# Kernel optimization log

Hardware: AMD Instinct MI355X
Metric: run time of the kernel (lower is better)

Reference implementation:

```python
import jax, jax.numpy as jnp
import numpy as np

B, F_SIZE, DIM = 2048, 32, 64
LAYER_SIZES = (128, 128)


def setup_inputs() -> dict:
    key = jax.random.key(0)
    k1, k2, k3 = jax.random.split(key, 3)
    inputs = jax.random.normal(k1, (B, F_SIZE, DIM), dtype=jnp.float32)
    # Conv1d(kernel=1) weights: (out_channels, in_channels)
    W0 = jax.random.normal(k2, (128, F_SIZE * F_SIZE), dtype=jnp.float32) * 0.03
    b0 = jnp.zeros((128,), dtype=jnp.float32)
    # split_half -> field_nums[1] = 64 -> in_channels = 64 * 32 = 2048
    W1 = jax.random.normal(k3, (128, 64 * F_SIZE), dtype=jnp.float32) * 0.03
    b1 = jnp.zeros((128,), dtype=jnp.float32)
    return {"inputs": inputs, "W0": W0, "b0": b0, "W1": W1, "b1": b1}


def _cin_forward(inputs, Ws, bs):
    batch, _, dim = inputs.shape
    x0 = inputs
    h = inputs
    finals = []
    n_layers = len(Ws)
    for i in range(n_layers):
        H = h.shape[1]
        M = x0.shape[1]
        # outer-product interaction: (b, H, M, d) -> (b, H*M, d)
        z = jnp.einsum('bhd,bmd->bhmd', h, x0).reshape(batch, H * M, dim)
        # 1x1 conv == per-position channel matmul
        out = jnp.einsum('bcd,oc->bod', z, Ws[i]) + bs[i][None, :, None]
        out = jax.nn.relu(out)
        size = Ws[i].shape[0]
        if i != n_layers - 1:
            # split_half: first half feeds next layer, second half is output
            h = out[:, : size // 2, :]
            finals.append(out[:, size // 2 :, :])
        else:
            finals.append(out)
    result = jnp.concatenate(finals, axis=1)  # (b, 64 + 128, d)
    return jnp.sum(result, axis=-1)           # (b, 192)


def reference(inputs, W0, b0, W1, b1):
    return _cin_forward(inputs, (W0, W1), (b0, b1))
```

## Files before the change

kernel.cpp:

```cpp
#include <hip/hip_runtime.h>


#define K0 1024
#define K1 2048
#define OUTC 192
#define L0_ELEMS (128 * K0)
#define L1_ELEMS (128 * K1)
#define L0_FRAGS (L0_ELEMS / 8)
#define L1_FRAGS (L1_ELEMS / 8)

typedef _Float16 v8h  __attribute__((ext_vector_type(8)));
typedef _Float16 v2h  __attribute__((ext_vector_type(2)));
typedef float    v16f __attribute__((ext_vector_type(16)));

__global__ void convert_w_kernel(const float* __restrict__ W0,
                                 const float* __restrict__ W1,
                                 _Float16* __restrict__ wsw) {
    int t = blockIdx.x * blockDim.x + threadIdx.x;
    if (t >= L0_FRAGS + L1_FRAGS) return;
    const float* src;
    _Float16* dst;
    if (t < L0_FRAGS) {
        int lane = t & 63, rt = (t >> 6) & 3, ks = t >> 8;
        int row = rt * 32 + (lane & 31);
        int k   = ks * 16 + (lane >> 5) * 8;
        src = W0 + (size_t)row * K0 + k;
        dst = wsw + (size_t)t * 8;
    } else {
        int u = t - L0_FRAGS;
        int lane = u & 63, rt = (u >> 6) & 3, ks = u >> 8;
        int row = rt * 32 + (lane & 31);
        int k   = ks * 16 + (lane >> 5) * 8;
        src = W1 + (size_t)row * K1 + k;
        dst = wsw + L0_ELEMS + (size_t)u * 8;
    }
    #pragma unroll
    for (int j = 0; j < 8; ++j) dst[j] = (_Float16)src[j];
}

__device__ __forceinline__ v8h dupscalar(uint32_t u) {
    uint32_t pair = (u << 16) | u;
    v2h p = __builtin_bit_cast(v2h, pair);
    return __builtin_shufflevector(p, p, 0, 1, 0, 1, 0, 1, 0, 1);
}

__global__ __launch_bounds__(256, 4) void cin_kernel(
    const float* __restrict__ X,
    const float* __restrict__ b0,
    const float* __restrict__ b1,
    const _Float16* __restrict__ Wsw,
    float* __restrict__ out)
{
    __shared__ uint16_t xS[2][32 * 64];
    __shared__ uint16_t h1S[2][64 * 64];
    __shared__ float biasLds[256];

    const int tid  = threadIdx.x;
    const int wave = tid >> 6;
    const int lane = tid & 63;
    const int bi   = wave >> 1;
    const int rw   = wave & 1;
    const int l31  = lane & 31;
    const int hi   = lane >> 5;
    const size_t bb = (size_t)blockIdx.x * 2;

    if (tid < 128) biasLds[tid] = b0[tid];
    else           biasLds[tid] = b1[tid - 128];

    const float* xsrc = X + bb * 2048;
    for (int i = tid; i < 4096; i += 256) {
        int bby = i >> 11, loc = i & 2047;
        int m = loc >> 6, d = loc & 63;
        _Float16 h = (_Float16)xsrc[i];
        ((_Float16*)&h1S[bby][0])[d * 40 + m] = h;
        xS[bby][m * 64 + d] = __builtin_bit_cast(uint16_t, h);
    }
    __syncthreads();

    v8h xv[2][2];
    {
        const _Float16* xT = (const _Float16*)&h1S[bi][0];
        #pragma unroll
        for (int c = 0; c < 2; ++c)
            #pragma unroll
            for (int p = 0; p < 2; ++p)
                xv[c][p] = *(const v8h*)&xT[(c * 32 + l31) * 40 + p * 16 + hi * 8];
    }
    __syncthreads();

    v16f acc[2][2];
    #pragma unroll
    for (int rt = 0; rt < 2; ++rt)
        #pragma unroll
        for (int c = 0; c < 2; ++c) acc[rt][c] = (v16f)0.0f;

    {
        const _Float16* Wp = Wsw + (size_t)rw * 1024 + (size_t)lane * 8;
        #pragma unroll 2
        for (int h = 0; h < 32; ++h) {
            v8h a00 = *(const v8h*)(Wp);
            v8h a10 = *(const v8h*)(Wp + 512);
            v8h a01 = *(const v8h*)(Wp + 2048);
            v8h a11 = *(const v8h*)(Wp + 2560);
            Wp += 4096;
            uint32_t u0 = xS[bi][h * 64 + l31];
            uint32_t u1 = xS[bi][h * 64 + 32 + l31];
            v8h s80 = dupscalar(u0), s81 = dupscalar(u1);
            v8h b00 = s80 * xv[0][0];
            acc[0][0] = __builtin_amdgcn_mfma_f32_32x32x16_f16(a00, b00, acc[0][0], 0, 0, 0);
            acc[1][0] = __builtin_amdgcn_mfma_f32_32x32x16_f16(a10, b00, acc[1][0], 0, 0, 0);
            v8h b10 = s81 * xv[1][0];
            acc[0][1] = __builtin_amdgcn_mfma_f32_32x32x16_f16(a00, b10, acc[0][1], 0, 0, 0);
            acc[1][1] = __builtin_amdgcn_mfma_f32_32x32x16_f16(a10, b10, acc[1][1], 0, 0, 0);
            v8h b01 = s80 * xv[0][1];
            acc[0][0] = __builtin_amdgcn_mfma_f32_32x32x16_f16(a01, b01, acc[0][0], 0, 0, 0);
            acc[1][0] = __builtin_amdgcn_mfma_f32_32x32x16_f16(a11, b01, acc[1][0], 0, 0, 0);
            v8h b11 = s81 * xv[1][1];
            acc[0][1] = __builtin_amdgcn_mfma_f32_32x32x16_f16(a01, b11, acc[0][1], 0, 0, 0);
            acc[1][1] = __builtin_amdgcn_mfma_f32_32x32x16_f16(a11, b11, acc[1][1], 0, 0, 0);
        }
    }

    if (rw == 0) {
        #pragma unroll
        for (int rt = 0; rt < 2; ++rt)
            #pragma unroll
            for (int reg = 0; reg < 16; ++reg) {
                int row = rt * 32 + (reg & 3) + 8 * (reg >> 2) + 4 * hi;
                float bias = biasLds[row];
                #pragma unroll
                for (int c = 0; c < 2; ++c) {
                    float v = acc[rt][c][reg] + bias;
                    v = v > 0.0f ? v : 0.0f;
                    h1S[bi][row * 64 + c * 32 + l31] =
                        __builtin_bit_cast(uint16_t, (_Float16)v);
                }
            }
    } else {
        #pragma unroll
        for (int rt = 0; rt < 2; ++rt)
            #pragma unroll
            for (int reg = 0; reg < 16; ++reg) {
                int grow = 64 + rt * 32 + (reg & 3) + 8 * (reg >> 2) + 4 * hi;
                float bias = biasLds[grow];
                float v0 = acc[rt][0][reg] + bias;
                float v1 = acc[rt][1][reg] + bias;
                float s = (v0 > 0.0f ? v0 : 0.0f) + (v1 > 0.0f ? v1 : 0.0f);
                s += __shfl_xor(s, 1);
                s += __shfl_xor(s, 2);
                s += __shfl_xor(s, 4);
                s += __shfl_xor(s, 8);
                s += __shfl_xor(s, 16);
                if (l31 == 0) out[(bb + bi) * OUTC + (grow - 64)] = s;
            }
    }
    __syncthreads();

    #pragma unroll
    for (int rt = 0; rt < 2; ++rt)
        #pragma unroll
        for (int c = 0; c < 2; ++c) acc[rt][c] = (v16f)0.0f;

    {
        const _Float16* Wp = Wsw + L0_ELEMS + (size_t)rw * 1024 + (size_t)lane * 8;
        #pragma unroll 2
        for (int h = 0; h < 64; ++h) {
            v8h a00 = *(const v8h*)(Wp);
            v8h a10 = *(const v8h*)(Wp + 512);
            v8h a01 = *(const v8h*)(Wp + 2048);
            v8h a11 = *(const v8h*)(Wp + 2560);
            Wp += 4096;
            uint32_t u0 = h1S[bi][h * 64 + l31];
            uint32_t u1 = h1S[bi][h * 64 + 32 + l31];
            v8h s80 = dupscalar(u0), s81 = dupscalar(u1);
            v8h b00 = s80 * xv[0][0];
            acc[0][0] = __builtin_amdgcn_mfma_f32_32x32x16_f16(a00, b00, acc[0][0], 0, 0, 0);
            acc[1][0] = __builtin_amdgcn_mfma_f32_32x32x16_f16(a10, b00, acc[1][0], 0, 0, 0);
            v8h b10 = s81 * xv[1][0];
            acc[0][1] = __builtin_amdgcn_mfma_f32_32x32x16_f16(a00, b10, acc[0][1], 0, 0, 0);
            acc[1][1] = __builtin_amdgcn_mfma_f32_32x32x16_f16(a10, b10, acc[1][1], 0, 0, 0);
            v8h b01 = s80 * xv[0][1];
            acc[0][0] = __builtin_amdgcn_mfma_f32_32x32x16_f16(a01, b01, acc[0][0], 0, 0, 0);
            acc[1][0] = __builtin_amdgcn_mfma_f32_32x32x16_f16(a11, b01, acc[1][0], 0, 0, 0);
            v8h b11 = s81 * xv[1][1];
            acc[0][1] = __builtin_amdgcn_mfma_f32_32x32x16_f16(a01, b11, acc[0][1], 0, 0, 0);
            acc[1][1] = __builtin_amdgcn_mfma_f32_32x32x16_f16(a11, b11, acc[1][1], 0, 0, 0);
        }
    }

    #pragma unroll
    for (int rt = 0; rt < 2; ++rt)
        #pragma unroll
        for (int reg = 0; reg < 16; ++reg) {
            int grow = rw * 64 + rt * 32 + (reg & 3) + 8 * (reg >> 2) + 4 * hi;
            float bias = biasLds[128 + grow];
            float v0 = acc[rt][0][reg] + bias;
            float v1 = acc[rt][1][reg] + bias;
            float s = (v0 > 0.0f ? v0 : 0.0f) + (v1 > 0.0f ? v1 : 0.0f);
            s += __shfl_xor(s, 1);
            s += __shfl_xor(s, 2);
            s += __shfl_xor(s, 4);
            s += __shfl_xor(s, 8);
            s += __shfl_xor(s, 16);
            if (l31 == 0) out[(bb + bi) * OUTC + 64 + grow] = s;
        }
}

extern "C" void kernel_launch(void* const* d_in, const int* in_sizes, int n_in,
                              void* d_out, int out_size, void* d_ws, size_t ws_size,
                              hipStream_t stream) {
    const float* X  = (const float*)d_in[0];
    const float* W0 = (const float*)d_in[1];
    const float* b0 = (const float*)d_in[2];
    const float* W1 = (const float*)d_in[3];
    const float* b1 = (const float*)d_in[4];
    float* out = (float*)d_out;
    _Float16* wsw = (_Float16*)d_ws;

    convert_w_kernel<<<(L0_FRAGS + L1_FRAGS + 255) / 256, 256, 0, stream>>>(W0, W1, wsw);
    cin_kernel<<<1024, 256, 0, stream>>>(X, b0, b1, wsw, out);
}
```

Measured before the change: 175.1 us.

## Process one batch per block with waves split by row tile and prefetch weights

Changes the work split from two batch items per block (each handled by two waves over 64 rows) to one batch item per block, with the four waves each owning a 32-row tile. Each wave now holds two accumulators instead of four. Weight fragments and LDS scalars are software-pipelined two iterations ahead in registers. This doubles the grid and halves per-wave accumulator registers, aiming for more parallelism and latency hiding. In exchange, each weight fragment is reused across only one batch item instead of two, which increases global/L2 weight traffic per output.

```diff
diff --git a/kernel.cpp b/kernel.cpp
--- a/kernel.cpp
+++ b/kernel.cpp
@@ -44,6 +44,8 @@
     return __builtin_shufflevector(p, p, 0, 1, 0, 1, 0, 1, 0, 1);
 }
 
+#define MFMA32(A, B, C) __builtin_amdgcn_mfma_f32_32x32x16_f16((A), (B), (C), 0, 0, 0)
+
 __global__ __launch_bounds__(256, 4) void cin_kernel(
     const float* __restrict__ X,
     const float* __restrict__ b0,
@@ -51,35 +53,32 @@
     const _Float16* __restrict__ Wsw,
     float* __restrict__ out)
 {
-    __shared__ uint16_t xS[2][32 * 64];
-    __shared__ uint16_t h1S[2][64 * 64];
+    __shared__ uint16_t xS[32 * 64];
+    __shared__ uint16_t h1S[64 * 64];
     __shared__ float biasLds[256];
 
     const int tid  = threadIdx.x;
     const int wave = tid >> 6;
     const int lane = tid & 63;
-    const int bi   = wave >> 1;
-    const int rw   = wave & 1;
     const int l31  = lane & 31;
     const int hi   = lane >> 5;
-    const size_t bb = (size_t)blockIdx.x * 2;
+    const size_t b = blockIdx.x;
 
     if (tid < 128) biasLds[tid] = b0[tid];
     else           biasLds[tid] = b1[tid - 128];
 
-    const float* xsrc = X + bb * 2048;
-    for (int i = tid; i < 4096; i += 256) {
-        int bby = i >> 11, loc = i & 2047;
-        int m = loc >> 6, d = loc & 63;
+    const float* xsrc = X + b * 2048;
+    for (int i = tid; i < 2048; i += 256) {
+        int m = i >> 6, d = i & 63;
         _Float16 h = (_Float16)xsrc[i];
-        ((_Float16*)&h1S[bby][0])[d * 40 + m] = h;
-        xS[bby][m * 64 + d] = __builtin_bit_cast(uint16_t, h);
+        ((_Float16*)h1S)[d * 40 + m] = h;
+        xS[m * 64 + d] = __builtin_bit_cast(uint16_t, h);
     }
     __syncthreads();
 
     v8h xv[2][2];
     {
-        const _Float16* xT = (const _Float16*)&h1S[bi][0];
+        const _Float16* xT = (const _Float16*)h1S;
         #pragma unroll
         for (int c = 0; c < 2; ++c)
             #pragma unroll
@@ -88,122 +87,110 @@
     }
     __syncthreads();
 
-    v16f acc[2][2];
-    #pragma unroll
-    for (int rt = 0; rt < 2; ++rt)
-        #pragma unroll
-        for (int c = 0; c < 2; ++c) acc[rt][c] = (v16f)0.0f;
-
+    v16f acc0 = (v16f)0.0f, acc1 = (v16f)0.0f;
     {
-        const _Float16* Wp = Wsw + (size_t)rw * 1024 + (size_t)lane * 8;
+        const _Float16* Wb = Wsw + (size_t)wave * 512 + (size_t)lane * 8;
+        v8h Ap0 = *(const v8h*)(Wb);
+        v8h Ap1 = *(const v8h*)(Wb + 2048);
+        v8h Bp0 = *(const v8h*)(Wb + 4096);
+        v8h Bp1 = *(const v8h*)(Wb + 4096 + 2048);
+        uint32_t ua0 = xS[l31],      ua1 = xS[32 + l31];
+        uint32_t ub0 = xS[64 + l31], ub1 = xS[64 + 32 + l31];
         #pragma unroll 2
         for (int h = 0; h < 32; ++h) {
-            v8h a00 = *(const v8h*)(Wp);
-            v8h a10 = *(const v8h*)(Wp + 512);
-            v8h a01 = *(const v8h*)(Wp + 2048);
-            v8h a11 = *(const v8h*)(Wp + 2560);
-            Wp += 4096;
-            uint32_t u0 = xS[bi][h * 64 + l31];
-            uint32_t u1 = xS[bi][h * 64 + 32 + l31];
-            v8h s80 = dupscalar(u0), s81 = dupscalar(u1);
+            int hn = (h + 2 < 32) ? h + 2 : 31;
+            v8h P0 = *(const v8h*)(Wb + (size_t)hn * 4096);
+            v8h P1 = *(const v8h*)(Wb + (size_t)hn * 4096 + 2048);
+            uint32_t w0 = xS[hn * 64 + l31];
+            uint32_t w1 = xS[hn * 64 + 32 + l31];
+            v8h s80 = dupscalar(ua0), s81 = dupscalar(ua1);
             v8h b00 = s80 * xv[0][0];
-            acc[0][0] = __builtin_amdgcn_mfma_f32_32x32x16_f16(a00, b00, acc[0][0], 0, 0, 0);
-            acc[1][0] = __builtin_amdgcn_mfma_f32_32x32x16_f16(a10, b00, acc[1][0], 0, 0, 0);
             v8h b10 = s81 * xv[1][0];
-            acc[0][1] = __builtin_amdgcn_mfma_f32_32x32x16_f16(a00, b10, acc[0][1], 0, 0, 0);
-            acc[1][1] = __builtin_amdgcn_mfma_f32_32x32x16_f16(a10, b10, acc[1][1], 0, 0, 0);
+            acc0 = MFMA32(Ap0, b00, acc0);
+            acc1 = MFMA32(Ap0, b10, acc1);
             v8h b01 = s80 * xv[0][1];
-            acc[0][0] = __builtin_amdgcn_mfma_f32_32x32x16_f16(a01, b01, acc[0][0], 0, 0, 0);
-            acc[1][0] = __builtin_amdgcn_mfma_f32_32x32x16_f16(a11, b01, acc[1][0], 0, 0, 0);
             v8h b11 = s81 * xv[1][1];
-            acc[0][1] = __builtin_amdgcn_mfma_f32_32x32x16_f16(a01, b11, acc[0][1], 0, 0, 0);
-            acc[1][1] = __builtin_amdgcn_mfma_f32_32x32x16_f16(a11, b11, acc[1][1], 0, 0, 0);
-        }
-    }
-
-    if (rw == 0) {
+            acc0 = MFMA32(Ap1, b01, acc0);
+            acc1 = MFMA32(Ap1, b11, acc1);
+            Ap0 = Bp0; Ap1 = Bp1; Bp0 = P0; Bp1 = P1;
+            ua0 = ub0; ua1 = ub1; ub0 = w0; ub1 = w1;
+        }
+    }
+
+    if (wave < 2) {
         #pragma unroll
-        for (int rt = 0; rt < 2; ++rt)
-            #pragma unroll
-            for (int reg = 0; reg < 16; ++reg) {
-                int row = rt * 32 + (reg & 3) + 8 * (reg >> 2) + 4 * hi;
-                float bias = biasLds[row];
-                #pragma unroll
-                for (int c = 0; c < 2; ++c) {
-                    float v = acc[rt][c][reg] + bias;
-                    v = v > 0.0f ? v : 0.0f;
-                    h1S[bi][row * 64 + c * 32 + l31] =
-                        __builtin_bit_cast(uint16_t, (_Float16)v);
-                }
-            }
+        for (int reg = 0; reg < 16; ++reg) {
+            int row = wave * 32 + (reg & 3) + 8 * (reg >> 2) + 4 * hi;
+            float bias = biasLds[row];
+            float v0 = acc0[reg] + bias;
+            float v1 = acc1[reg] + bias;
+            v0 = v0 > 0.0f ? v0 : 0.0f;
+            v1 = v1 > 0.0f ? v1 : 0.0f;
+            h1S[row * 64 + l31]      = __builtin_bit_cast(uint16_t, (_Float16)v0);
+            h1S[row * 64 + 32 + l31] = __builtin_bit_cast(uint16_t, (_Float16)v1);
+        }
     } else {
         #pragma unroll
-        for (int rt = 0; rt < 2; ++rt)
-            #pragma unroll
-            for (int reg = 0; reg < 16; ++reg) {
-                int grow = 64 + rt * 32 + (reg & 3) + 8 * (reg >> 2) + 4 * hi;
-                float bias = biasLds[grow];
-                float v0 = acc[rt][0][reg] + bias;
-                float v1 = acc[rt][1][reg] + bias;
-                float s = (v0 > 0.0f ? v0 : 0.0f) + (v1 > 0.0f ? v1 : 0.0f);
-                s += __shfl_xor(s, 1);
-                s += __shfl_xor(s, 2);
-                s += __shfl_xor(s, 4);
-                s += __shfl_xor(s, 8);
-                s += __shfl_xor(s, 16);
-                if (l31 == 0) out[(bb + bi) * OUTC + (grow - 64)] = s;
-            }
-    }
-    __syncthreads();
-
-    #pragma unroll
-    for (int rt = 0; rt < 2; ++rt)
-        #pragma unroll
-        for (int c = 0; c < 2; ++c) acc[rt][c] = (v16f)0.0f;
-
-    {
-        const _Float16* Wp = Wsw + L0_ELEMS + (size_t)rw * 1024 + (size_t)lane * 8;
-        #pragma unroll 2
-        for (int h = 0; h < 64; ++h) {
-            v8h a00 = *(const v8h*)(Wp);
-            v8h a10 = *(const v8h*)(Wp + 512);
-            v8h a01 = *(const v8h*)(Wp + 2048);
-            v8h a11 = *(const v8h*)(Wp + 2560);
-            Wp += 4096;
-            uint32_t u0 = h1S[bi][h * 64 + l31];
-            uint32_t u1 = h1S[bi][h * 64 + 32 + l31];
-            v8h s80 = dupscalar(u0), s81 = dupscalar(u1);
-            v8h b00 = s80 * xv[0][0];
-            acc[0][0] = __builtin_amdgcn_mfma_f32_32x32x16_f16(a00, b00, acc[0][0], 0, 0, 0);
-            acc[1][0] = __builtin_amdgcn_mfma_f32_32x32x16_f16(a10, b00, acc[1][0], 0, 0, 0);
-            v8h b10 = s81 * xv[1][0];
-            acc[0][1] = __builtin_amdgcn_mfma_f32_32x32x16_f16(a00, b10, acc[0][1], 0, 0, 0);
-            acc[1][1] = __builtin_amdgcn_mfma_f32_32x32x16_f16(a10, b10, acc[1][1], 0, 0, 0);
-            v8h b01 = s80 * xv[0][1];
-            acc[0][0] = __builtin_amdgcn_mfma_f32_32x32x16_f16(a01, b01, acc[0][0], 0, 0, 0);
-            acc[1][0] = __builtin_amdgcn_mfma_f32_32x32x16_f16(a11, b01, acc[1][0], 0, 0, 0);
-            v8h b11 = s81 * xv[1][1];
-            acc[0][1] = __builtin_amdgcn_mfma_f32_32x32x16_f16(a01, b11, acc[0][1], 0, 0, 0);
-            acc[1][1] = __builtin_amdgcn_mfma_f32_32x32x16_f16(a11, b11, acc[1][1], 0, 0, 0);
-        }
-    }
-
-    #pragma unroll
-    for (int rt = 0; rt < 2; ++rt)
-        #pragma unroll
         for (int reg = 0; reg < 16; ++reg) {
-            int grow = rw * 64 + rt * 32 + (reg & 3) + 8 * (reg >> 2) + 4 * hi;
-            float bias = biasLds[128 + grow];
-            float v0 = acc[rt][0][reg] + bias;
-            float v1 = acc[rt][1][reg] + bias;
+            int grow = wave * 32 + (reg & 3) + 8 * (reg >> 2) + 4 * hi;
+            float bias = biasLds[grow];
+            float v0 = acc0[reg] + bias;
+            float v1 = acc1[reg] + bias;
             float s = (v0 > 0.0f ? v0 : 0.0f) + (v1 > 0.0f ? v1 : 0.0f);
             s += __shfl_xor(s, 1);
             s += __shfl_xor(s, 2);
             s += __shfl_xor(s, 4);
             s += __shfl_xor(s, 8);
             s += __shfl_xor(s, 16);
-            if (l31 == 0) out[(bb + bi) * OUTC + 64 + grow] = s;
-        }
+            if (l31 == 0) out[b * OUTC + (grow - 64)] = s;
+        }
+    }
+    __syncthreads();
+
+    acc0 = (v16f)0.0f; acc1 = (v16f)0.0f;
+    {
+        const _Float16* Wb = Wsw + L0_ELEMS + (size_t)wave * 512 + (size_t)lane * 8;
+        v8h Ap0 = *(const v8h*)(Wb);
+        v8h Ap1 = *(const v8h*)(Wb + 2048);
+        v8h Bp0 = *(const v8h*)(Wb + 4096);
+        v8h Bp1 = *(const v8h*)(Wb + 4096 + 2048);
+        uint32_t ua0 = h1S[l31],      ua1 = h1S[32 + l31];
+        uint32_t ub0 = h1S[64 + l31], ub1 = h1S[64 + 32 + l31];
+        #pragma unroll 2
+        for (int h = 0; h < 64; ++h) {
+            int hn = (h + 2 < 64) ? h + 2 : 63;
+            v8h P0 = *(const v8h*)(Wb + (size_t)hn * 4096);
+            v8h P1 = *(const v8h*)(Wb + (size_t)hn * 4096 + 2048);
+            uint32_t w0 = h1S[hn * 64 + l31];
+            uint32_t w1 = h1S[hn * 64 + 32 + l31];
+            v8h s80 = dupscalar(ua0), s81 = dupscalar(ua1);
+            v8h b00 = s80 * xv[0][0];
+            v8h b10 = s81 * xv[1][0];
+            acc0 = MFMA32(Ap0, b00, acc0);
+            acc1 = MFMA32(Ap0, b10, acc1);
+            v8h b01 = s80 * xv[0][1];
+            v8h b11 = s81 * xv[1][1];
+            acc0 = MFMA32(Ap1, b01, acc0);
+            acc1 = MFMA32(Ap1, b11, acc1);
+            Ap0 = Bp0; Ap1 = Bp1; Bp0 = P0; Bp1 = P1;
+            ua0 = ub0; ua1 = ub1; ub0 = w0; ub1 = w1;
+        }
+    }
+
+    #pragma unroll
+    for (int reg = 0; reg < 16; ++reg) {
+        int grow = wave * 32 + (reg & 3) + 8 * (reg >> 2) + 4 * hi;
+        float bias = biasLds[128 + grow];
+        float v0 = acc0[reg] + bias;
+        float v1 = acc1[reg] + bias;
+        float s = (v0 > 0.0f ? v0 : 0.0f) + (v1 > 0.0f ? v1 : 0.0f);
+        s += __shfl_xor(s, 1);
+        s += __shfl_xor(s, 2);
+        s += __shfl_xor(s, 4);
+        s += __shfl_xor(s, 8);
+        s += __shfl_xor(s, 16);
+        if (l31 == 0) out[b * OUTC + 64 + grow] = s;
+    }
 }
 
 extern "C" void kernel_launch(void* const* d_in, const int* in_sizes, int n_in,
@@ -218,5 +205,5 @@
     _Float16* wsw = (_Float16*)d_ws;
 
     convert_w_kernel<<<(L0_FRAGS + L1_FRAGS + 255) / 256, 256, 0, stream>>>(W0, W1, wsw);
-    cin_kernel<<<1024, 256, 0, stream>>>(X, b0, b1, wsw, out);
-}
+    cin_kernel<<<2048, 256, 0, stream>>>(X, b0, b1, wsw, out);
+}
```

New measurement: 177.6 us. About the same (+1.4%).

## Process two batch samples per wave to reuse weight fragments, prefetch next iteration

Applied to the files above, without the earlier changes.

Each block now handles four batch samples instead of two, and each wave computes two samples so every weight fragment loaded from global memory feeds twice as many MFMAs. The K loops are software-pipelined so the next iteration's weight and LDS scalar loads are issued before the current MFMAs. The conversion kernel is reindexed to read source rows contiguously. Accumulator registers double and launch bounds drop to 2 blocks per SIMD, so occupancy falls and the grid is halved.

```diff
diff --git a/kernel.cpp b/kernel.cpp
--- a/kernel.cpp
+++ b/kernel.cpp
@@ -6,8 +6,6 @@
 #define OUTC 192
 #define L0_ELEMS (128 * K0)
 #define L1_ELEMS (128 * K1)
-#define L0_FRAGS (L0_ELEMS / 8)
-#define L1_FRAGS (L1_ELEMS / 8)
 
 typedef _Float16 v8h  __attribute__((ext_vector_type(8)));
 typedef _Float16 v2h  __attribute__((ext_vector_type(2)));
@@ -16,26 +14,23 @@
 __global__ void convert_w_kernel(const float* __restrict__ W0,
                                  const float* __restrict__ W1,
                                  _Float16* __restrict__ wsw) {
-    int t = blockIdx.x * blockDim.x + threadIdx.x;
-    if (t >= L0_FRAGS + L1_FRAGS) return;
+    size_t i = ((size_t)blockIdx.x * blockDim.x + threadIdx.x) * 8;
+    if (i >= (size_t)(L0_ELEMS + L1_ELEMS)) return;
     const float* src;
-    _Float16* dst;
-    if (t < L0_FRAGS) {
-        int lane = t & 63, rt = (t >> 6) & 3, ks = t >> 8;
-        int row = rt * 32 + (lane & 31);
-        int k   = ks * 16 + (lane >> 5) * 8;
-        src = W0 + (size_t)row * K0 + k;
-        dst = wsw + (size_t)t * 8;
+    _Float16* dstbase;
+    int K, local;
+    if (i < L0_ELEMS) {
+        K = K0; src = W0; dstbase = wsw; local = (int)i;
     } else {
-        int u = t - L0_FRAGS;
-        int lane = u & 63, rt = (u >> 6) & 3, ks = u >> 8;
-        int row = rt * 32 + (lane & 31);
-        int k   = ks * 16 + (lane >> 5) * 8;
-        src = W1 + (size_t)row * K1 + k;
-        dst = wsw + L0_ELEMS + (size_t)u * 8;
-    }
-    #pragma unroll
-    for (int j = 0; j < 8; ++j) dst[j] = (_Float16)src[j];
+        K = K1; src = W1; dstbase = wsw + L0_ELEMS; local = (int)(i - L0_ELEMS);
+    }
+    int row = local / K, k = local % K;
+    int ks = k >> 4, oct = (k >> 3) & 1;
+    int frag = ks * 256 + (row >> 5) * 64 + oct * 32 + (row & 31);
+    const float* s = src + (size_t)row * K + k;
+    _Float16* d = dstbase + (size_t)frag * 8;
+    #pragma unroll
+    for (int j = 0; j < 8; ++j) d[j] = (_Float16)s[j];
 }
 
 __device__ __forceinline__ v8h dupscalar(uint32_t u) {
@@ -44,31 +39,34 @@
     return __builtin_shufflevector(p, p, 0, 1, 0, 1, 0, 1, 0, 1);
 }
 
-__global__ __launch_bounds__(256, 4) void cin_kernel(
+#define MFMA32(A, B, C) __builtin_amdgcn_mfma_f32_32x32x16_f16((A), (B), (C), 0, 0, 0)
+
+__global__ __launch_bounds__(256, 2) void cin_kernel(
     const float* __restrict__ X,
     const float* __restrict__ b0,
     const float* __restrict__ b1,
     const _Float16* __restrict__ Wsw,
     float* __restrict__ out)
 {
-    __shared__ uint16_t xS[2][32 * 64];
-    __shared__ uint16_t h1S[2][64 * 64];
+    __shared__ uint16_t xS[4][2048];
+    __shared__ uint16_t h1S[4][4096];
     __shared__ float biasLds[256];
 
     const int tid  = threadIdx.x;
     const int wave = tid >> 6;
     const int lane = tid & 63;
-    const int bi   = wave >> 1;
     const int rw   = wave & 1;
+    const int bp   = wave >> 1;
+    const int lb0  = bp * 2;
     const int l31  = lane & 31;
     const int hi   = lane >> 5;
-    const size_t bb = (size_t)blockIdx.x * 2;
+    const size_t bb = (size_t)blockIdx.x * 4;
 
     if (tid < 128) biasLds[tid] = b0[tid];
     else           biasLds[tid] = b1[tid - 128];
 
     const float* xsrc = X + bb * 2048;
-    for (int i = tid; i < 4096; i += 256) {
+    for (int i = tid; i < 8192; i += 256) {
         int bby = i >> 11, loc = i & 2047;
         int m = loc >> 6, d = loc & 63;
         _Float16 h = (_Float16)xsrc[i];
@@ -77,133 +75,244 @@
     }
     __syncthreads();
 
-    v8h xv[2][2];
-    {
-        const _Float16* xT = (const _Float16*)&h1S[bi][0];
+    v8h xv[2][2][2];
+    #pragma unroll
+    for (int lb = 0; lb < 2; ++lb) {
+        const _Float16* xT = (const _Float16*)&h1S[lb0 + lb][0];
         #pragma unroll
         for (int c = 0; c < 2; ++c)
             #pragma unroll
             for (int p = 0; p < 2; ++p)
-                xv[c][p] = *(const v8h*)&xT[(c * 32 + l31) * 40 + p * 16 + hi * 8];
+                xv[lb][c][p] = *(const v8h*)&xT[(c * 32 + l31) * 40 + p * 16 + hi * 8];
     }
     __syncthreads();
 
-    v16f acc[2][2];
-    #pragma unroll
-    for (int rt = 0; rt < 2; ++rt)
-        #pragma unroll
-        for (int c = 0; c < 2; ++c) acc[rt][c] = (v16f)0.0f;
+    v16f acc[2][2][2];
+    #pragma unroll
+    for (int lb = 0; lb < 2; ++lb)
+        #pragma unroll
+        for (int rt = 0; rt < 2; ++rt)
+            #pragma unroll
+            for (int c = 0; c < 2; ++c) acc[lb][rt][c] = (v16f)0.0f;
 
     {
         const _Float16* Wp = Wsw + (size_t)rw * 1024 + (size_t)lane * 8;
+        const uint16_t* xp0 = &xS[lb0][0];
+        const uint16_t* xp1 = &xS[lb0 + 1][0];
+        v8h na00 = *(const v8h*)(Wp);
+        v8h na10 = *(const v8h*)(Wp + 512);
+        v8h na01 = *(const v8h*)(Wp + 2048);
+        v8h na11 = *(const v8h*)(Wp + 2560);
+        uint32_t nu00 = xp0[l31], nu01 = xp0[32 + l31];
+        uint32_t nu10 = xp1[l31], nu11 = xp1[32 + l31];
         #pragma unroll 2
-        for (int h = 0; h < 32; ++h) {
-            v8h a00 = *(const v8h*)(Wp);
-            v8h a10 = *(const v8h*)(Wp + 512);
-            v8h a01 = *(const v8h*)(Wp + 2048);
-            v8h a11 = *(const v8h*)(Wp + 2560);
+        for (int h = 0; h < 31; ++h) {
+            v8h a00 = na00, a10 = na10, a01 = na01, a11 = na11;
+            uint32_t u00 = nu00, u01 = nu01, u10 = nu10, u11 = nu11;
             Wp += 4096;
-            uint32_t u0 = xS[bi][h * 64 + l31];
-            uint32_t u1 = xS[bi][h * 64 + 32 + l31];
-            v8h s80 = dupscalar(u0), s81 = dupscalar(u1);
-            v8h b00 = s80 * xv[0][0];
-            acc[0][0] = __builtin_amdgcn_mfma_f32_32x32x16_f16(a00, b00, acc[0][0], 0, 0, 0);
-            acc[1][0] = __builtin_amdgcn_mfma_f32_32x32x16_f16(a10, b00, acc[1][0], 0, 0, 0);
-            v8h b10 = s81 * xv[1][0];
-            acc[0][1] = __builtin_amdgcn_mfma_f32_32x32x16_f16(a00, b10, acc[0][1], 0, 0, 0);
-            acc[1][1] = __builtin_amdgcn_mfma_f32_32x32x16_f16(a10, b10, acc[1][1], 0, 0, 0);
-            v8h b01 = s80 * xv[0][1];
-            acc[0][0] = __builtin_amdgcn_mfma_f32_32x32x16_f16(a01, b01, acc[0][0], 0, 0, 0);
-            acc[1][0] = __builtin_amdgcn_mfma_f32_32x32x16_f16(a11, b01, acc[1][0], 0, 0, 0);
-            v8h b11 = s81 * xv[1][1];
-            acc[0][1] = __builtin_amdgcn_mfma_f32_32x32x16_f16(a01, b11, acc[0][1], 0, 0, 0);
-            acc[1][1] = __builtin_amdgcn_mfma_f32_32x32x16_f16(a11, b11, acc[1][1], 0, 0, 0);
+            na00 = *(const v8h*)(Wp);
+            na10 = *(const v8h*)(Wp + 512);
+            na01 = *(const v8h*)(Wp + 2048);
+            na11 = *(const v8h*)(Wp + 2560);
+            nu00 = xp0[(h + 1) * 64 + l31];
+            nu01 = xp0[(h + 1) * 64 + 32 + l31];
+            nu10 = xp1[(h + 1) * 64 + l31];
+            nu11 = xp1[(h + 1) * 64 + 32 + l31];
+            v8h s00 = dupscalar(u00), s01 = dupscalar(u01);
+            v8h s10 = dupscalar(u10), s11 = dupscalar(u11);
+            v8h b000 = s00 * xv[0][0][0];
+            acc[0][0][0] = MFMA32(a00, b000, acc[0][0][0]);
+            acc[0][1][0] = MFMA32(a10, b000, acc[0][1][0]);
+            v8h b010 = s01 * xv[0][1][0];
+            acc[0][0][1] = MFMA32(a00, b010, acc[0][0][1]);
+            acc[0][1][1] = MFMA32(a10, b010, acc[0][1][1]);
+            v8h b100 = s10 * xv[1][0][0];
+            acc[1][0][0] = MFMA32(a00, b100, acc[1][0][0]);
+            acc[1][1][0] = MFMA32(a10, b100, acc[1][1][0]);
+            v8h b110 = s11 * xv[1][1][0];
+            acc[1][0][1] = MFMA32(a00, b110, acc[1][0][1]);
+            acc[1][1][1] = MFMA32(a10, b110, acc[1][1][1]);
+            v8h b001 = s00 * xv[0][0][1];
+            acc[0][0][0] = MFMA32(a01, b001, acc[0][0][0]);
+            acc[0][1][0] = MFMA32(a11, b001, acc[0][1][0]);
+            v8h b011 = s01 * xv[0][1][1];
+            acc[0][0][1] = MFMA32(a01, b011, acc[0][0][1]);
+            acc[0][1][1] = MFMA32(a11, b011, acc[0][1][1]);
+            v8h b101 = s10 * xv[1][0][1];
+            acc[1][0][0] = MFMA32(a01, b101, acc[1][0][0]);
+            acc[1][1][0] = MFMA32(a11, b101, acc[1][1][0]);
+            v8h b111 = s11 * xv[1][1][1];
+            acc[1][0][1] = MFMA32(a01, b111, acc[1][0][1]);
+            acc[1][1][1] = MFMA32(a11, b111, acc[1][1][1]);
         }
+        v8h s00 = dupscalar(nu00), s01 = dupscalar(nu01);
+        v8h s10 = dupscalar(nu10), s11 = dupscalar(nu11);
+        v8h b000 = s00 * xv[0][0][0];
+        acc[0][0][0] = MFMA32(na00, b000, acc[0][0][0]);
+        acc[0][1][0] = MFMA32(na10, b000, acc[0][1][0]);
+        v8h b010 = s01 * xv[0][1][0];
+        acc[0][0][1] = MFMA32(na00, b010, acc[0][0][1]);
+        acc[0][1][1] = MFMA32(na10, b010, acc[0][1][1]);
+        v8h b100 = s10 * xv[1][0][0];
+        acc[1][0][0] = MFMA32(na00, b100, acc[1][0][0]);
+        acc[1][1][0] = MFMA32(na10, b100, acc[1][1][0]);
+        v8h b110 = s11 * xv[1][1][0];
+        acc[1][0][1] = MFMA32(na00, b110, acc[1][0][1]);
+        acc[1][1][1] = MFMA32(na10, b110, acc[1][1][1]);
+        v8h b001 = s00 * xv[0][0][1];
+        acc[0][0][0] = MFMA32(na01, b001, acc[0][0][0]);
+        acc[0][1][0] = MFMA32(na11, b001, acc[0][1][0]);
+        v8h b011 = s01 * xv[0][1][1];
+        acc[0][0][1] = MFMA32(na01, b011, acc[0][0][1]);
+        acc[0][1][1] = MFMA32(na11, b011, acc[0][1][1]);
+        v8h b101 = s10 * xv[1][0][1];
+        acc[1][0][0] = MFMA32(na01, b101, acc[1][0][0]);
+        acc[1][1][0] = MFMA32(na11, b101, acc[1][1][0]);
+        v8h b111 = s11 * xv[1][1][1];
+        acc[1][0][1] = MFMA32(na01, b111, acc[1][0][1]);
+        acc[1][1][1] = MFMA32(na11, b111, acc[1][1][1]);
     }
 
     if (rw == 0) {
         #pragma unroll
+        for (int lb = 0; lb < 2; ++lb)
+            #pragma unroll
+            for (int rt = 0; rt < 2; ++rt)
+                #pragma unroll
+                for (int reg = 0; reg < 16; ++reg) {
+                    int row = rt * 32 + (reg & 3) + 8 * (reg >> 2) + 4 * hi;
+                    float bias = biasLds[row];
+                    float v0 = acc[lb][rt][0][reg] + bias;
+                    float v1 = acc[lb][rt][1][reg] + bias;
+                    v0 = v0 > 0.0f ? v0 : 0.0f;
+                    v1 = v1 > 0.0f ? v1 : 0.0f;
+                    h1S[lb0 + lb][row * 64 + l31]      = __builtin_bit_cast(uint16_t, (_Float16)v0);
+                    h1S[lb0 + lb][row * 64 + 32 + l31] = __builtin_bit_cast(uint16_t, (_Float16)v1);
+                }
+    } else {
+        #pragma unroll
+        for (int lb = 0; lb < 2; ++lb)
+            #pragma unroll
+            for (int rt = 0; rt < 2; ++rt)
+                #pragma unroll
+                for (int reg = 0; reg < 16; ++reg) {
+                    int grow = 64 + rt * 32 + (reg & 3) + 8 * (reg >> 2) + 4 * hi;
+                    float bias = biasLds[grow];
+                    float v0 = acc[lb][rt][0][reg] + bias;
+                    float v1 = acc[lb][rt][1][reg] + bias;
+                    float s = (v0 > 0.0f ? v0 : 0.0f) + (v1 > 0.0f ? v1 : 0.0f);
+                    s += __shfl_xor(s, 1);
+                    s += __shfl_xor(s, 2);
+                    s += __shfl_xor(s, 4);
+                    s += __shfl_xor(s, 8);
+                    s += __shfl_xor(s, 16);
+                    if (l31 == 0) out[(bb + lb0 + lb) * OUTC + (grow - 64)] = s;
+                }
+    }
+    __syncthreads();
+
+    #pragma unroll
+    for (int lb = 0; lb < 2; ++lb)
+        #pragma unroll
         for (int rt = 0; rt < 2; ++rt)
             #pragma unroll
+            for (int c = 0; c < 2; ++c) acc[lb][rt][c] = (v16f)0.0f;
+    {
+        const _Float16* Wp = Wsw + L0_ELEMS + (size_t)rw * 1024 + (size_t)lane * 8;
+        const uint16_t* hp0 = &h1S[lb0][0];
+        const uint16_t* hp1 = &h1S[lb0 + 1][0];
+        v8h na00 = *(const v8h*)(Wp);
+        v8h na10 = *(const v8h*)(Wp + 512);
+        v8h na01 = *(const v8h*)(Wp + 2048);
+        v8h na11 = *(const v8h*)(Wp + 2560);
+        uint32_t nu00 = hp0[l31], nu01 = hp0[32 + l31];
+        uint32_t nu10 = hp1[l31], nu11 = hp1[32 + l31];
+        #pragma unroll 2
+        for (int h = 0; h < 63; ++h) {
+            v8h a00 = na00, a10 = na10, a01 = na01, a11 = na11;
+            uint32_t u00 = nu00, u01 = nu01, u10 = nu10, u11 = nu11;
+            Wp += 4096;
+            na00 = *(const v8h*)(Wp);
+            na10 = *(const v8h*)(Wp + 512);
+            na01 = *(const v8h*)(Wp + 2048);
+            na11 = *(const v8h*)(Wp + 2560);
+            nu00 = hp0[(h + 1) * 64 + l31];
+            nu01 = hp0[(h + 1) * 64 + 32 + l31];
+            nu10 = hp1[(h + 1) * 64 + l31];
+            nu11 = hp1[(h + 1) * 64 + 32 + l31];
+            v8h s00 = dupscalar(u00), s01 = dupscalar(u01);
+            v8h s10 = dupscalar(u10), s11 = dupscalar(u11);
+            v8h b000 = s00 * xv[0][0][0];
+            acc[0][0][0] = MFMA32(a00, b000, acc[0][0][0]);
+            acc[0][1][0] = MFMA32(a10, b000, acc[0][1][0]);
+            v8h b010 = s01 * xv[0][1][0];
+            acc[0][0][1] = MFMA32(a00, b010, acc[0][0][1]);
+            acc[0][1][1] = MFMA32(a10, b010, acc[0][1][1]);
+            v8h b100 = s10 * xv[1][0][0];
+            acc[1][0][0] = MFMA32(a00, b100, acc[1][0][0]);
+            acc[1][1][0] = MFMA32(a10, b100, acc[1][1][0]);
+            v8h b110 = s11 * xv[1][1][0];
+            acc[1][0][1] = MFMA32(a00, b110, acc[1][0][1]);
+            acc[1][1][1] = MFMA32(a10, b110, acc[1][1][1]);
+            v8h b001 = s00 * xv[0][0][1];
+            acc[0][0][0] = MFMA32(a01, b001, acc[0][0][0]);
+            acc[0][1][0] = MFMA32(a11, b001, acc[0][1][0]);
+            v8h b011 = s01 * xv[0][1][1];
+            acc[0][0][1] = MFMA32(a01, b011, acc[0][0][1]);
+            acc[0][1][1] = MFMA32(a11, b011, acc[0][1][1]);
+            v8h b101 = s10 * xv[1][0][1];
+            acc[1][0][0] = MFMA32(a01, b101, acc[1][0][0]);
+            acc[1][1][0] = MFMA32(a11, b101, acc[1][1][0]);
+            v8h b111 = s11 * xv[1][1][1];
+            acc[1][0][1] = MFMA32(a01, b111, acc[1][0][1]);
+            acc[1][1][1] = MFMA32(a11, b111, acc[1][1][1]);
+        }
+        v8h s00 = dupscalar(nu00), s01 = dupscalar(nu01);
+        v8h s10 = dupscalar(nu10), s11 = dupscalar(nu11);
+        v8h b000 = s00 * xv[0][0][0];
+        acc[0][0][0] = MFMA32(na00, b000, acc[0][0][0]);
+        acc[0][1][0] = MFMA32(na10, b000, acc[0][1][0]);
+        v8h b010 = s01 * xv[0][1][0];
+        acc[0][0][1] = MFMA32(na00, b010, acc[0][0][1]);
+        acc[0][1][1] = MFMA32(na10, b010, acc[0][1][1]);
+        v8h b100 = s10 * xv[1][0][0];
+        acc[1][0][0] = MFMA32(na00, b100, acc[1][0][0]);
+        acc[1][1][0] = MFMA32(na10, b100, acc[1][1][0]);
+        v8h b110 = s11 * xv[1][1][0];
+        acc[1][0][1] = MFMA32(na00, b110, acc[1][0][1]);
+        acc[1][1][1] = MFMA32(na10, b110, acc[1][1][1]);
+        v8h b001 = s00 * xv[0][0][1];
+        acc[0][0][0] = MFMA32(na01, b001, acc[0][0][0]);
+        acc[0][1][0] = MFMA32(na11, b001, acc[0][1][0]);
+        v8h b011 = s01 * xv[0][1][1];
+        acc[0][0][1] = MFMA32(na01, b011, acc[0][0][1]);
+        acc[0][1][1] = MFMA32(na11, b011, acc[0][1][1]);
+        v8h b101 = s10 * xv[1][0][1];
+        acc[1][0][0] = MFMA32(na01, b101, acc[1][0][0]);
+        acc[1][1][0] = MFMA32(na11, b101, acc[1][1][0]);
+        v8h b111 = s11 * xv[1][1][1];
+        acc[1][0][1] = MFMA32(na01, b111, acc[1][0][1]);
+        acc[1][1][1] = MFMA32(na11, b111, acc[1][1][1]);
+    }
+
+    #pragma unroll
+    for (int lb = 0; lb < 2; ++lb)
+        #pragma unroll
+        for (int rt = 0; rt < 2; ++rt)
+            #pragma unroll
             for (int reg = 0; reg < 16; ++reg) {
-                int row = rt * 32 + (reg & 3) + 8 * (reg >> 2) + 4 * hi;
-                float bias = biasLds[row];
-                #pragma unroll
-                for (int c = 0; c < 2; ++c) {
-                    float v = acc[rt][c][reg] + bias;
-                    v = v > 0.0f ? v : 0.0f;
-                    h1S[bi][row * 64 + c * 32 + l31] =
-                        __builtin_bit_cast(uint16_t, (_Float16)v);
-                }
-            }
-    } else {
-        #pragma unroll
-        for (int rt = 0; rt < 2; ++rt)
-            #pragma unroll
-            for (int reg = 0; reg < 16; ++reg) {
-                int grow = 64 + rt * 32 + (reg & 3) + 8 * (reg >> 2) + 4 * hi;
-                float bias = biasLds[grow];
-                float v0 = acc[rt][0][reg] + bias;
-                float v1 = acc[rt][1][reg] + bias;
+                int grow = rw * 64 + rt * 32 + (reg & 3) + 8 * (reg >> 2) + 4 * hi;
+                float bias = biasLds[128 + grow];
+                float v0 = acc[lb][rt][0][reg] + bias;
+                float v1 = acc[lb][rt][1][reg] + bias;
                 float s = (v0 > 0.0f ? v0 : 0.0f) + (v1 > 0.0f ? v1 : 0.0f);
                 s += __shfl_xor(s, 1);
                 s += __shfl_xor(s, 2);
                 s += __shfl_xor(s, 4);
                 s += __shfl_xor(s, 8);
                 s += __shfl_xor(s, 16);
-                if (l31 == 0) out[(bb + bi) * OUTC + (grow - 64)] = s;
+                if (l31 == 0) out[(bb + lb0 + lb) * OUTC + 64 + grow] = s;
             }
-    }
-    __syncthreads();
-
-    #pragma unroll
-    for (int rt = 0; rt < 2; ++rt)
-        #pragma unroll
-        for (int c = 0; c < 2; ++c) acc[rt][c] = (v16f)0.0f;
-
-    {
-        const _Float16* Wp = Wsw + L0_ELEMS + (size_t)rw * 1024 + (size_t)lane * 8;
-        #pragma unroll 2
-        for (int h = 0; h < 64; ++h) {
-            v8h a00 = *(const v8h*)(Wp);
-            v8h a10 = *(const v8h*)(Wp + 512);
-            v8h a01 = *(const v8h*)(Wp + 2048);
-            v8h a11 = *(const v8h*)(Wp + 2560);
-            Wp += 4096;
-            uint32_t u0 = h1S[bi][h * 64 + l31];
-            uint32_t u1 = h1S[bi][h * 64 + 32 + l31];
-            v8h s80 = dupscalar(u0), s81 = dupscalar(u1);
-            v8h b00 = s80 * xv[0][0];
-            acc[0][0] = __builtin_amdgcn_mfma_f32_32x32x16_f16(a00, b00, acc[0][0], 0, 0, 0);
-            acc[1][0] = __builtin_amdgcn_mfma_f32_32x32x16_f16(a10, b00, acc[1][0], 0, 0, 0);
-            v8h b10 = s81 * xv[1][0];
-            acc[0][1] = __builtin_amdgcn_mfma_f32_32x32x16_f16(a00, b10, acc[0][1], 0, 0, 0);
-            acc[1][1] = __builtin_amdgcn_mfma_f32_32x32x16_f16(a10, b10, acc[1][1], 0, 0, 0);
-            v8h b01 = s80 * xv[0][1];
-            acc[0][0] = __builtin_amdgcn_mfma_f32_32x32x16_f16(a01, b01, acc[0][0], 0, 0, 0);
-            acc[1][0] = __builtin_amdgcn_mfma_f32_32x32x16_f16(a11, b01, acc[1][0], 0, 0, 0);
-            v8h b11 = s81 * xv[1][1];
-            acc[0][1] = __builtin_amdgcn_mfma_f32_32x32x16_f16(a01, b11, acc[0][1], 0, 0, 0);
-            acc[1][1] = __builtin_amdgcn_mfma_f32_32x32x16_f16(a11, b11, acc[1][1], 0, 0, 0);
-        }
-    }
-
-    #pragma unroll
-    for (int rt = 0; rt < 2; ++rt)
-        #pragma unroll
-        for (int reg = 0; reg < 16; ++reg) {
-            int grow = rw * 64 + rt * 32 + (reg & 3) + 8 * (reg >> 2) + 4 * hi;
-            float bias = biasLds[128 + grow];
-            float v0 = acc[rt][0][reg] + bias;
-            float v1 = acc[rt][1][reg] + bias;
-            float s = (v0 > 0.0f ? v0 : 0.0f) + (v1 > 0.0f ? v1 : 0.0f);
-            s += __shfl_xor(s, 1);
-            s += __shfl_xor(s, 2);
-            s += __shfl_xor(s, 4);
-            s += __shfl_xor(s, 8);
-            s += __shfl_xor(s, 16);
-            if (l31 == 0) out[(bb + bi) * OUTC + 64 + grow] = s;
-        }
 }
 
 extern "C" void kernel_launch(void* const* d_in, const int* in_sizes, int n_in,
@@ -217,6 +326,7 @@
     float* out = (float*)d_out;
     _Float16* wsw = (_Float16*)d_ws;
 
-    convert_w_kernel<<<(L0_FRAGS + L1_FRAGS + 255) / 256, 256, 0, stream>>>(W0, W1, wsw);
-    cin_kernel<<<1024, 256, 0, stream>>>(X, b0, b1, wsw, out);
+    int nconv = (L0_ELEMS + L1_ELEMS) / 8;
+    convert_w_kernel<<<(nconv + 255) / 256, 256, 0, stream>>>(W0, W1, wsw);
+    cin_kernel<<<512, 256, 0, stream>>>(X, b0, b1, wsw, out);
 }
```

Measured after the change: 176.4 us. No clear change (+0.7%).
